# Kernel optimization log

Measured on AMD Instinct MI355X. Metric: run time of the kernel, lower is better.

The kernel has to match this reference:

```python
import jax, jax.numpy as jnp
import numpy as np

B, S, D, H = 2, 2048, 1024, 16
HD = D // H  # head_dim = 64


def setup_inputs() -> dict:
    key = jax.random.key(0)
    ks = jax.random.split(key, 9)
    scale = 0.02
    x = jax.random.normal(ks[0], (B, S, D), dtype=jnp.float32)
    wq = jax.random.normal(ks[1], (D, D), dtype=jnp.float32) * scale
    bq = jnp.zeros((D,), dtype=jnp.float32)
    wk = jax.random.normal(ks[2], (D, D), dtype=jnp.float32) * scale
    bk = jnp.zeros((D,), dtype=jnp.float32)
    wv = jax.random.normal(ks[3], (D, D), dtype=jnp.float32) * scale
    bv = jnp.zeros((D,), dtype=jnp.float32)
    wo = jax.random.normal(ks[4], (D, D), dtype=jnp.float32) * scale
    bo = jnp.zeros((D,), dtype=jnp.float32)
    # causal mask: 1.0 where key position is in the future of query position
    mask = jnp.triu(jnp.ones((S, S), dtype=jnp.float32), k=1)[None, None]  # [1,1,S,S]
    return {"x": x, "wq": wq, "bq": bq, "wk": wk, "bk": bk,
            "wv": wv, "bv": bv, "wo": wo, "bo": bo, "mask": mask}


def reference(x, wq, bq, wk, bk, wv, bv, wo, bo, mask):
    b, s, d = x.shape
    q = (x @ wq + bq).reshape(b, s, H, HD).transpose(0, 2, 1, 3)  # [b,h,s,hd]
    k = (x @ wk + bk).reshape(b, s, H, HD).transpose(0, 2, 1, 3)
    v = (x @ wv + bv).reshape(b, s, H, HD).transpose(0, 2, 1, 3)
    scores = jnp.einsum('bhqd,bhkd->bhqk', q, k) / jnp.sqrt(jnp.float32(HD))
    scores = scores + mask * (-1e9)
    probs = jax.nn.softmax(scores, axis=-1)
    out = jnp.einsum('bhqk,bhkd->bhqd', probs, v)
    out = out.transpose(0, 2, 1, 3).reshape(b, s, d)
    return out @ wo + bo
```

## Files before the change

kernel.cpp:

```cpp
#include <hip/hip_runtime.h>
#include <hip/hip_bf16.h>
#include <cstdint>

#define DEV static __device__ __forceinline__

typedef unsigned short u16t;
typedef __attribute__((ext_vector_type(4))) float f32x4;
typedef __attribute__((ext_vector_type(4))) unsigned short u16x4;
typedef __attribute__((ext_vector_type(8))) unsigned short u16x8;
typedef __attribute__((ext_vector_type(8))) __bf16 bf16x8;

DEV u16t f2bf(float f) {
  unsigned u = __builtin_bit_cast(unsigned, f);
  u += 0x7fffu + ((u >> 16) & 1u);
  return (u16t)(u >> 16);
}
DEV float bf2f(u16t h) {
  unsigned u = ((unsigned)h) << 16;
  return __builtin_bit_cast(float, u);
}

DEV void gload_lds16(const void* g, void* l) {
  __builtin_amdgcn_global_load_lds(
      (const __attribute__((address_space(1))) void*)g,
      (__attribute__((address_space(3))) void*)l, 16, 0, 0);
}

DEV bf16x8 ldsfrag(const u16t* p) {
  return __builtin_bit_cast(bf16x8, *(const u16x8*)p);
}

DEV void bsync() {
  asm volatile("" ::: "memory");
  __builtin_amdgcn_s_barrier();
  asm volatile("" ::: "memory");
}

__global__ __launch_bounds__(256) void k_convert_x(const float* __restrict__ x,
                                                   u16t* __restrict__ xb) {
  int i = (blockIdx.x * 256 + threadIdx.x) * 4;
  f32x4 v = *(const f32x4*)&x[i];
  u16x4 o;
#pragma unroll
  for (int j = 0; j < 4; ++j) o[j] = f2bf(v[j]);
  *(u16x4*)&xb[i] = o;
}

__global__ __launch_bounds__(256) void k_transw(const float* __restrict__ w0,
                                                const float* __restrict__ w1,
                                                const float* __restrict__ w2,
                                                const float* __restrict__ w3,
                                                u16t* __restrict__ qkvT,
                                                u16t* __restrict__ oT) {
  __shared__ float lds[64][68];
  int z = blockIdx.z;
  const float* W = (z == 0) ? w0 : (z == 1) ? w1 : (z == 2) ? w2 : w3;
  u16t* OUT = (z < 3) ? (qkvT + (size_t)z * 1024 * 1024) : oT;
  int k0 = blockIdx.x * 64, n0 = blockIdx.y * 64;
  int t = threadIdx.x;
  int kl = t >> 4, n4 = (t & 15) << 2;
#pragma unroll
  for (int p = 0; p < 4; ++p) {
    f32x4 v = *(const f32x4*)&W[(size_t)(k0 + kl + p * 16) * 1024 + n0 + n4];
    *(f32x4*)&lds[kl + p * 16][n4] = v;
  }
  __syncthreads();
  int nl = t >> 4, k4 = (t & 15) << 2;
#pragma unroll
  for (int p = 0; p < 4; ++p) {
    int n = nl + p * 16;
    u16x4 o;
#pragma unroll
    for (int i = 0; i < 4; ++i) o[i] = f2bf(lds[k4 + i][n]);
    *(u16x4*)&OUT[(size_t)(n0 + n) * 1024 + k0 + k4] = o;
  }
}

template <int MI, bool BF16_OUT, bool VSPLIT>
__global__ __launch_bounds__(256) void k_gemm_bt(const u16t* __restrict__ A,
                                                 const u16t* __restrict__ BT,
                                                 void* __restrict__ Cout,
                                                 const float* __restrict__ b0,
                                                 const float* __restrict__ b1,
                                                 const float* __restrict__ b2,
                                                 u16t* __restrict__ vt,
                                                 int M, int N, int K) {
  __shared__ u16t Al[2][MI * 32 * 64];
  __shared__ u16t Bl[2][128 * 64];
  const int tid = threadIdx.x;
  const int l = tid & 63;
  const int w = tid >> 6;
  const int m0 = blockIdx.x * (MI * 32), n0 = blockIdx.y * 128;
  const int wm = (w >> 1) * (MI * 16), wn = (w & 1) * 64;
  const int lm = l & 15, lh = l >> 4;
  f32x4 acc[MI][4] = {};

  auto stage = [&](int bb, int t) {
    const int k0 = t << 6;
#pragma unroll
    for (int s = 0; s < MI; ++s) {
      int c = s * 256 + tid;
      int row = c >> 3, slot = c & 7;
      int ks = k0 + (((slot ^ (row & 7)) & 7) << 3);
      gload_lds16(A + (size_t)(m0 + row) * K + ks, &Al[bb][c * 8]);
    }
#pragma unroll
    for (int s = 0; s < 4; ++s) {
      int c = s * 256 + tid;
      int row = c >> 3, slot = c & 7;
      int ks = k0 + (((slot ^ (row & 7)) & 7) << 3);
      gload_lds16(BT + (size_t)(n0 + row) * K + ks, &Bl[bb][c * 8]);
    }
  };

  const int nt = K >> 6;
  stage(0, 0);
  for (int t = 0; t < nt; ++t) {
    if (t + 1 < nt) {
      stage((t + 1) & 1, t + 1);
      if (MI == 2)
        asm volatile("s_waitcnt vmcnt(6)" ::: "memory");
      else
        asm volatile("s_waitcnt vmcnt(8)" ::: "memory");
    } else {
      asm volatile("s_waitcnt vmcnt(0)" ::: "memory");
    }
    bsync();
    const int buf = t & 1;

#pragma unroll
    for (int kk = 0; kk < 2; ++kk) {
      bf16x8 af[MI], bfr[4];
#pragma unroll
      for (int i = 0; i < MI; ++i) {
        int ra = wm + i * 16 + lm;
        int sa = (kk * 4 + lh) ^ (ra & 7);
        af[i] = ldsfrag(&Al[buf][ra * 64 + sa * 8]);
      }
#pragma unroll
      for (int i = 0; i < 4; ++i) {
        int rb = wn + i * 16 + lm;
        int sb = (kk * 4 + lh) ^ (rb & 7);
        bfr[i] = ldsfrag(&Bl[buf][rb * 64 + sb * 8]);
      }
#pragma unroll
      for (int i = 0; i < MI; ++i)
#pragma unroll
        for (int j = 0; j < 4; ++j)
          acc[i][j] = __builtin_amdgcn_mfma_f32_16x16x32_bf16(af[i], bfr[j],
                                                              acc[i][j], 0, 0, 0);
    }
    bsync();
  }

  if (!VSPLIT || (n0 + wn) < 2048) {
#pragma unroll
    for (int i = 0; i < MI; ++i) {
      int row = m0 + wm + i * 16 + (lh << 2);
#pragma unroll
      for (int j = 0; j < 4; ++j) {
        int col = n0 + wn + j * 16 + lm;
        const float* bp = (col < 1024) ? b0 : ((col < 2048) ? b1 : b2);
        float bias = bp[col & 1023];
#pragma unroll
        for (int r = 0; r < 4; ++r) {
          float v = acc[i][j][r] + bias;
          if (BF16_OUT)
            ((u16t*)Cout)[(size_t)(row + r) * N + col] = f2bf(v);
          else
            ((float*)Cout)[(size_t)(row + r) * N + col] = v;
        }
      }
    }
  } else {
#pragma unroll
    for (int i = 0; i < MI; ++i) {
      int row = m0 + wm + i * 16 + (lh << 2);
      int bidx = row >> 11, s0 = row & 2047;
#pragma unroll
      for (int j = 0; j < 4; ++j) {
        int col = n0 + wn + j * 16 + lm;
        int d = col - 2048;
        int hh = d >> 6, dd = d & 63;
        float bias = b2[d];
        u16x4 o;
#pragma unroll
        for (int r = 0; r < 4; ++r) o[r] = f2bf(acc[i][j][r] + bias);
        *(u16x4*)&vt[((size_t)((bidx * 16 + hh) * 64 + dd)) * 2048 + s0] = o;
      }
    }
  }
}

__global__ __launch_bounds__(256, 2) void k_attn(const u16t* qkv,
                                                 const u16t* __restrict__ vt,
                                                 u16t* __restrict__ outp,
                                                 u16t* scratch) {
  __shared__ u16t Kl[4096];
  __shared__ u16t Vl[4096];
  __shared__ u16t Pl[4][2][1024];
  const int tid = threadIdx.x, l = tid & 63, w = tid >> 6;
  const int lm = l & 15, lh = l >> 4;
  const int bh = blockIdx.x, b = bh >> 4, h = bh & 15;
  const int y = blockIdx.y;
  const int zone = y >> 3, j = y & 7;
  const int qt = (zone == 0) ? j : (15 - j);
  const int q0 = qt * 128;
  const int halfn = qt + 1;
  const int t0 = (zone == 2) ? halfn : 0;
  const int t1 = (zone == 1) ? halfn : (2 * qt + 2);
  const int qbase = q0 + w * 32;

  bf16x8 aq[2][2];
#pragma unroll
  for (int qm = 0; qm < 2; ++qm)
#pragma unroll
    for (int kk = 0; kk < 2; ++kk) {
      const u16t* src = qkv + (size_t)(b * 2048 + qbase + qm * 16 + lm) * 3072 +
                        h * 64 + kk * 32 + lh * 8;
      u16x8 v = *(const u16x8*)src;
      u16x8 o;
#pragma unroll
      for (int e = 0; e < 8; ++e) o[e] = f2bf(bf2f(v[e]) * 0.1803368801f);
      aq[qm][kk] = __builtin_bit_cast(bf16x8, o);
    }

  float lsum[2] = {0.f, 0.f};
  f32x4 aco[2][4] = {};
  const int qr0 = qbase + lm, qr1 = qbase + 16 + lm;

  const u16t* Kg = qkv + (size_t)b * 2048 * 3072 + 1024 + h * 64;
  const u16t* Vg = vt + (size_t)bh * 64 * 2048;

  auto stage = [&](int t) {
#pragma unroll
    for (int s = 0; s < 2; ++s) {
      int c = s * 256 + tid;
      int row = c >> 3, col = ((c & 7) ^ (row & 7)) << 3;
      gload_lds16(Kg + (size_t)(t * 64 + row) * 3072 + col, &Kl[c * 8]);
    }
#pragma unroll
    for (int s = 0; s < 2; ++s) {
      int c = s * 256 + tid;
      int row = c >> 3, col = ((c & 7) ^ (row & 7)) << 3;
      gload_lds16(Vg + (size_t)row * 2048 + t * 64 + col, &Vl[c * 8]);
    }
  };

  for (int t = t0; t < t1; ++t) {
    stage(t);
    asm volatile("s_waitcnt vmcnt(0)" ::: "memory");
    bsync();

    if (t * 64 <= qbase + 31) {
      f32x4 accs[2][4] = {};
#pragma unroll
      for (int kk = 0; kk < 2; ++kk) {
        bf16x8 ak[4];
#pragma unroll
        for (int nk = 0; nk < 4; ++nk) {
          int rk = nk * 16 + lm;
          int s16 = (kk * 4 + lh) ^ (rk & 7);
          ak[nk] = ldsfrag(&Kl[rk * 64 + s16 * 8]);
        }
        __builtin_amdgcn_s_setprio(1);
#pragma unroll
        for (int nk = 0; nk < 4; ++nk) {
          accs[0][nk] = __builtin_amdgcn_mfma_f32_16x16x32_bf16(
              ak[nk], aq[0][kk], accs[0][nk], 0, 0, 0);
          accs[1][nk] = __builtin_amdgcn_mfma_f32_16x16x32_bf16(
              ak[nk], aq[1][kk], accs[1][nk], 0, 0, 0);
        }
        __builtin_amdgcn_s_setprio(0);
      }

      if (t * 64 + 63 > qbase) {
#pragma unroll
        for (int nk = 0; nk < 4; ++nk)
#pragma unroll
          for (int r = 0; r < 4; ++r) {
            int kvpos = t * 64 + nk * 16 + lh * 4 + r;
            if (kvpos > qr0) accs[0][nk][r] = -1e30f;
            if (kvpos > qr1) accs[1][nk][r] = -1e30f;
          }
      }

#pragma unroll
      for (int qm = 0; qm < 2; ++qm) {
        u16t* Pw = &Pl[w][qm][0];
#pragma unroll
        for (int nk = 0; nk < 4; ++nk) {
          float p0 = exp2f(accs[qm][nk][0]);
          float p1 = exp2f(accs[qm][nk][1]);
          float p2 = exp2f(accs[qm][nk][2]);
          float p3 = exp2f(accs[qm][nk][3]);
          lsum[qm] += (p0 + p1) + (p2 + p3);
          unsigned wlo, whi;
          asm("v_cvt_pk_bf16_f32 %0, %1, %2" : "=v"(wlo) : "v"(p0), "v"(p1));
          asm("v_cvt_pk_bf16_f32 %0, %1, %2" : "=v"(whi) : "v"(p2), "v"(p3));
          int off = lm * 64 + ((((2 * nk + (lh >> 1)) ^ (lm & 7)) & 7) << 3) +
                    ((lh & 1) << 2);
          *(uint2*)&Pw[off] = make_uint2(wlo, whi);
        }
      }

#pragma unroll
      for (int kk = 0; kk < 2; ++kk) {
        int sp = (kk * 4 + lh) ^ (lm & 7);
        bf16x8 ap0 = ldsfrag(&Pl[w][0][lm * 64 + sp * 8]);
        bf16x8 ap1 = ldsfrag(&Pl[w][1][lm * 64 + sp * 8]);
        __builtin_amdgcn_s_setprio(1);
#pragma unroll
        for (int nd = 0; nd < 4; ++nd) {
          int rv = nd * 16 + lm;
          int sv = (kk * 4 + lh) ^ (rv & 7);
          bf16x8 bv = ldsfrag(&Vl[rv * 64 + sv * 8]);
          aco[0][nd] =
              __builtin_amdgcn_mfma_f32_16x16x32_bf16(ap0, bv, aco[0][nd], 0, 0, 0);
          aco[1][nd] =
              __builtin_amdgcn_mfma_f32_16x16x32_bf16(ap1, bv, aco[1][nd], 0, 0, 0);
        }
        __builtin_amdgcn_s_setprio(0);
      }
    }

    bsync();
  }

#pragma unroll
  for (int qm = 0; qm < 2; ++qm) {
    lsum[qm] += __shfl_xor(lsum[qm], 16);
    lsum[qm] += __shfl_xor(lsum[qm], 32);
  }

  if (zone == 0) {
#pragma unroll
    for (int qm = 0; qm < 2; ++qm) {
      float inv = 1.0f / lsum[qm];
#pragma unroll
      for (int r = 0; r < 4; ++r) {
        float ir = __shfl(inv, lh * 4 + r);
        int row = qbase + qm * 16 + lh * 4 + r;
#pragma unroll
        for (int nd = 0; nd < 4; ++nd) {
          int col = h * 64 + nd * 16 + lm;
          outp[(size_t)(b * 2048 + row) * 1024 + col] = f2bf(aco[qm][nd][r] * ir);
        }
      }
    }
  } else {
#pragma unroll
    for (int qm = 0; qm < 2; ++qm)
#pragma unroll
      for (int r = 0; r < 4; ++r) {
        int row = qbase + qm * 16 + lh * 4 + r;
#pragma unroll
        for (int nd = 0; nd < 4; ++nd) {
          int col = nd * 16 + lm;
          u16t v = f2bf(aco[qm][nd][r]);
          if (zone == 1)
            outp[(size_t)(b * 2048 + row) * 1024 + h * 64 + col] = v;
          else
            scratch[(size_t)(b * 2048 + row - 1024) * 3072 + 2048 + h * 64 + col] = v;
        }
      }
    if (l < 16) {
      float* ml0 = (float*)&scratch[(size_t)(b * 2048 + qbase + l) * 3072 + 2048];
      ml0[h * 2 + (zone - 1)] = lsum[0];
      float* ml1 =
          (float*)&scratch[(size_t)(b * 2048 + qbase + 16 + l) * 3072 + 2048];
      ml1[h * 2 + (zone - 1)] = lsum[1];
    }
  }
}

__global__ __launch_bounds__(256) void k_merge(const u16t* __restrict__ scratch,
                                               u16t* __restrict__ outp) {
  int x = blockIdx.x;
  int b = x >> 10, rr = x & 1023, row = 1024 + rr;
  int c4 = threadIdx.x * 4;
  int h = c4 >> 6;
  const float* ml = (const float*)&scratch[(size_t)(b * 2048 + row) * 3072 + 2048];
  float inv = 1.0f / (ml[h * 2] + ml[h * 2 + 1]);
  u16t* op = &outp[(size_t)(b * 2048 + row) * 1024 + c4];
  const u16t* o1 = &scratch[(size_t)(b * 2048 + rr) * 3072 + 2048 + c4];
  u16x4 a = *(const u16x4*)op;
  u16x4 bb = *(const u16x4*)o1;
  u16x4 o;
#pragma unroll
  for (int i = 0; i < 4; ++i) o[i] = f2bf((bf2f(a[i]) + bf2f(bb[i])) * inv);
  *(u16x4*)op = o;
}

extern "C" void kernel_launch(void* const* d_in, const int* in_sizes, int n_in,
                              void* d_out, int out_size, void* d_ws, size_t ws_size,
                              hipStream_t stream) {
  const float* x = (const float*)d_in[0];
  const float* wq = (const float*)d_in[1];
  const float* bq = (const float*)d_in[2];
  const float* wk = (const float*)d_in[3];
  const float* bk = (const float*)d_in[4];
  const float* wv = (const float*)d_in[5];
  const float* bv = (const float*)d_in[6];
  const float* wo = (const float*)d_in[7];
  const float* bo = (const float*)d_in[8];

  char* ws = (char*)d_ws;
  u16t* xb = (u16t*)ws;
  u16t* wqkvT = (u16t*)(ws + (8u << 20));
  u16t* woT = (u16t*)(ws + (14u << 20));
  u16t* qkv = (u16t*)(ws + (16u << 20));
  u16t* vt = (u16t*)(ws + (40u << 20));
  u16t* attn_out = xb;

  k_convert_x<<<4096, 256, 0, stream>>>(x, xb);
  k_transw<<<dim3(16, 16, 4), 256, 0, stream>>>(wq, wk, wv, wo, wqkvT, woT);
  k_gemm_bt<2, true, true><<<dim3(64, 24), 256, 0, stream>>>(
      xb, wqkvT, qkv, bq, bk, bv, vt, 4096, 3072, 1024);
  k_attn<<<dim3(32, 24), 256, 0, stream>>>(qkv, vt, attn_out, qkv);
  k_merge<<<2048, 256, 0, stream>>>(qkv, attn_out);
  k_gemm_bt<2, false, false><<<dim3(64, 8), 256, 0, stream>>>(
      attn_out, woT, d_out, bo, bo, bo, nullptr, 4096, 1024, 1024);
}
```

Measured before the change: 107.7 us.

## Add dedicated QKV GEMM kernel with 64x256 tiles and MFMA priority boost

Replaces the generic templated GEMM for the QKV projection with a specialized kernel using 64x256 block tiles (each wave computes 32x128), single-buffered LDS staging, and s_setprio around the MFMA loop. The wider N tile raises arithmetic intensity per A load and halves the grid to 768 blocks. The generic GEMM is simplified to fp32 output only. Dropping double buffering exposes global load latency each K step, and the larger accumulator footprint may reduce occupancy.

```diff
diff --git a/kernel.cpp b/kernel.cpp
--- a/kernel.cpp
+++ b/kernel.cpp
@@ -76,14 +76,100 @@
   }
 }
 
-template <int MI, bool BF16_OUT, bool VSPLIT>
+__global__ __launch_bounds__(256) void k_gemm_qkv(const u16t* __restrict__ A,
+                                                  const u16t* __restrict__ BT,
+                                                  u16t* __restrict__ Cout,
+                                                  const float* __restrict__ b0,
+                                                  const float* __restrict__ b1,
+                                                  const float* __restrict__ b2,
+                                                  u16t* __restrict__ vt) {
+  __shared__ u16t Al[64 * 64];
+  __shared__ u16t Bl[256 * 64];
+  const int tid = threadIdx.x;
+  const int l = tid & 63;
+  const int w = tid >> 6;
+  const int m0 = blockIdx.x * 64, n0 = blockIdx.y * 256;
+  const int wm = (w >> 1) * 32, wn = (w & 1) * 128;
+  const int lm = l & 15, lh = l >> 4;
+  f32x4 acc[2][8] = {};
+
+  for (int t = 0; t < 16; ++t) {
+    const int k0 = t << 6;
+#pragma unroll
+    for (int s = 0; s < 2; ++s) {
+      int c = s * 256 + tid;
+      int row = c >> 3, slot = c & 7;
+      int ks = k0 + (((slot ^ (row & 7)) & 7) << 3);
+      gload_lds16(A + (size_t)(m0 + row) * 1024 + ks, &Al[c * 8]);
+    }
+#pragma unroll
+    for (int s = 0; s < 8; ++s) {
+      int c = s * 256 + tid;
+      int row = c >> 3, slot = c & 7;
+      int ks = k0 + (((slot ^ (row & 7)) & 7) << 3);
+      gload_lds16(BT + (size_t)(n0 + row) * 1024 + ks, &Bl[c * 8]);
+    }
+    asm volatile("s_waitcnt vmcnt(0)" ::: "memory");
+    bsync();
+
+#pragma unroll
+    for (int kk = 0; kk < 2; ++kk) {
+      bf16x8 af[2], bfr[8];
+#pragma unroll
+      for (int i = 0; i < 2; ++i) {
+        int ra = wm + i * 16 + lm;
+        int sa = (kk * 4 + lh) ^ (ra & 7);
+        af[i] = ldsfrag(&Al[ra * 64 + sa * 8]);
+      }
+#pragma unroll
+      for (int j = 0; j < 8; ++j) {
+        int rb = wn + j * 16 + lm;
+        int sb = (kk * 4 + lh) ^ (rb & 7);
+        bfr[j] = ldsfrag(&Bl[rb * 64 + sb * 8]);
+      }
+      __builtin_amdgcn_s_setprio(1);
+#pragma unroll
+      for (int i = 0; i < 2; ++i)
+#pragma unroll
+        for (int j = 0; j < 8; ++j)
+          acc[i][j] = __builtin_amdgcn_mfma_f32_16x16x32_bf16(af[i], bfr[j],
+                                                              acc[i][j], 0, 0, 0);
+      __builtin_amdgcn_s_setprio(0);
+    }
+    bsync();
+  }
+
+#pragma unroll
+  for (int i = 0; i < 2; ++i) {
+    int row = m0 + wm + i * 16 + (lh << 2);
+    int bidx = row >> 11, s0 = row & 2047;
+#pragma unroll
+    for (int j = 0; j < 8; ++j) {
+      int col = n0 + wn + j * 16 + lm;
+      if (col < 2048) {
+        const float* bp = (col < 1024) ? b0 : b1;
+        float bias = bp[col & 1023];
+#pragma unroll
+        for (int r = 0; r < 4; ++r)
+          Cout[(size_t)(row + r) * 3072 + col] = f2bf(acc[i][j][r] + bias);
+      } else {
+        int d = col - 2048;
+        int hh = d >> 6, dd = d & 63;
+        float bias = b2[d];
+        u16x4 o;
+#pragma unroll
+        for (int r = 0; r < 4; ++r) o[r] = f2bf(acc[i][j][r] + bias);
+        *(u16x4*)&vt[((size_t)((bidx * 16 + hh) * 64 + dd)) * 2048 + s0] = o;
+      }
+    }
+  }
+}
+
+template <int MI>
 __global__ __launch_bounds__(256) void k_gemm_bt(const u16t* __restrict__ A,
                                                  const u16t* __restrict__ BT,
-                                                 void* __restrict__ Cout,
+                                                 float* __restrict__ Cout,
                                                  const float* __restrict__ b0,
-                                                 const float* __restrict__ b1,
-                                                 const float* __restrict__ b2,
-                                                 u16t* __restrict__ vt,
                                                  int M, int N, int K) {
   __shared__ u16t Al[2][MI * 32 * 64];
   __shared__ u16t Bl[2][128 * 64];
@@ -153,41 +239,16 @@
     bsync();
   }
 
-  if (!VSPLIT || (n0 + wn) < 2048) {
-#pragma unroll
-    for (int i = 0; i < MI; ++i) {
-      int row = m0 + wm + i * 16 + (lh << 2);
-#pragma unroll
-      for (int j = 0; j < 4; ++j) {
-        int col = n0 + wn + j * 16 + lm;
-        const float* bp = (col < 1024) ? b0 : ((col < 2048) ? b1 : b2);
-        float bias = bp[col & 1023];
-#pragma unroll
-        for (int r = 0; r < 4; ++r) {
-          float v = acc[i][j][r] + bias;
-          if (BF16_OUT)
-            ((u16t*)Cout)[(size_t)(row + r) * N + col] = f2bf(v);
-          else
-            ((float*)Cout)[(size_t)(row + r) * N + col] = v;
-        }
-      }
-    }
-  } else {
-#pragma unroll
-    for (int i = 0; i < MI; ++i) {
-      int row = m0 + wm + i * 16 + (lh << 2);
-      int bidx = row >> 11, s0 = row & 2047;
-#pragma unroll
-      for (int j = 0; j < 4; ++j) {
-        int col = n0 + wn + j * 16 + lm;
-        int d = col - 2048;
-        int hh = d >> 6, dd = d & 63;
-        float bias = b2[d];
-        u16x4 o;
-#pragma unroll
-        for (int r = 0; r < 4; ++r) o[r] = f2bf(acc[i][j][r] + bias);
-        *(u16x4*)&vt[((size_t)((bidx * 16 + hh) * 64 + dd)) * 2048 + s0] = o;
-      }
+#pragma unroll
+  for (int i = 0; i < MI; ++i) {
+    int row = m0 + wm + i * 16 + (lh << 2);
+#pragma unroll
+    for (int j = 0; j < 4; ++j) {
+      int col = n0 + wn + j * 16 + lm;
+      float bias = b0[col];
+#pragma unroll
+      for (int r = 0; r < 4; ++r)
+        Cout[(size_t)(row + r) * N + col] = acc[i][j][r] + bias;
     }
   }
 }
@@ -415,10 +476,9 @@
 
   k_convert_x<<<4096, 256, 0, stream>>>(x, xb);
   k_transw<<<dim3(16, 16, 4), 256, 0, stream>>>(wq, wk, wv, wo, wqkvT, woT);
-  k_gemm_bt<2, true, true><<<dim3(64, 24), 256, 0, stream>>>(
-      xb, wqkvT, qkv, bq, bk, bv, vt, 4096, 3072, 1024);
+  k_gemm_qkv<<<dim3(64, 12), 256, 0, stream>>>(xb, wqkvT, qkv, bq, bk, bv, vt);
   k_attn<<<dim3(32, 24), 256, 0, stream>>>(qkv, vt, attn_out, qkv);
   k_merge<<<2048, 256, 0, stream>>>(qkv, attn_out);
-  k_gemm_bt<2, false, false><<<dim3(64, 8), 256, 0, stream>>>(
-      attn_out, woT, d_out, bo, bo, bo, nullptr, 4096, 1024, 1024);
-}
+  k_gemm_bt<2><<<dim3(64, 8), 256, 0, stream>>>(attn_out, woT, (float*)d_out, bo,
+                                                4096, 1024, 1024);
+}
```

New measurement: 122.6 us. 13.9% more time.

## Keep P in registers and compute transposed PV with 16x16x16 MFMA

Applied to the files above, without the earlier changes.

The P tile no longer round-trips through shared memory. The score accumulator layout is fed straight in as the B operand of a 16x16x16 bf16 MFMA, with V as the A operand, which produces a transposed output accumulator. The epilogue then writes contiguous 4-element vectors per row, replacing the scattered scalar stores and removing the shuffle for the normaliser. In exchange it uses the smaller-K MFMA (twice as many instructions for the PV product) and narrower 8-byte V fragment reads from LDS, but drops the LDS writes and reads of P and frees that LDS space.

```diff
diff --git a/kernel.cpp b/kernel.cpp
--- a/kernel.cpp
+++ b/kernel.cpp
@@ -9,6 +9,7 @@
 typedef __attribute__((ext_vector_type(4))) unsigned short u16x4;
 typedef __attribute__((ext_vector_type(8))) unsigned short u16x8;
 typedef __attribute__((ext_vector_type(8))) __bf16 bf16x8;
+typedef __attribute__((ext_vector_type(4))) short s16x4;
 
 DEV u16t f2bf(float f) {
   unsigned u = __builtin_bit_cast(unsigned, f);
@@ -198,7 +199,6 @@
                                                  u16t* scratch) {
   __shared__ u16t Kl[4096];
   __shared__ u16t Vl[4096];
-  __shared__ u16t Pl[4][2][1024];
   const int tid = threadIdx.x, l = tid & 63, w = tid >> 6;
   const int lm = l & 15, lh = l >> 4;
   const int bh = blockIdx.x, b = bh >> 4, h = bh & 15;
@@ -226,7 +226,7 @@
     }
 
   float lsum[2] = {0.f, 0.f};
-  f32x4 aco[2][4] = {};
+  f32x4 acoT[2][4] = {};
   const int qr0 = qbase + lm, qr1 = qbase + 16 + lm;
 
   const u16t* Kg = qkv + (size_t)b * 2048 * 3072 + 1024 + h * 64;
@@ -285,9 +285,9 @@
           }
       }
 
-#pragma unroll
-      for (int qm = 0; qm < 2; ++qm) {
-        u16t* Pw = &Pl[w][qm][0];
+      s16x4 pb[2][4];
+#pragma unroll
+      for (int qm = 0; qm < 2; ++qm)
 #pragma unroll
         for (int nk = 0; nk < 4; ++nk) {
           float p0 = exp2f(accs[qm][nk][0]);
@@ -298,27 +298,26 @@
           unsigned wlo, whi;
           asm("v_cvt_pk_bf16_f32 %0, %1, %2" : "=v"(wlo) : "v"(p0), "v"(p1));
           asm("v_cvt_pk_bf16_f32 %0, %1, %2" : "=v"(whi) : "v"(p2), "v"(p3));
-          int off = lm * 64 + ((((2 * nk + (lh >> 1)) ^ (lm & 7)) & 7) << 3) +
-                    ((lh & 1) << 2);
-          *(uint2*)&Pw[off] = make_uint2(wlo, whi);
-        }
-      }
-
-#pragma unroll
-      for (int kk = 0; kk < 2; ++kk) {
-        int sp = (kk * 4 + lh) ^ (lm & 7);
-        bf16x8 ap0 = ldsfrag(&Pl[w][0][lm * 64 + sp * 8]);
-        bf16x8 ap1 = ldsfrag(&Pl[w][1][lm * 64 + sp * 8]);
+          pb[qm][nk] = __builtin_bit_cast(s16x4, make_uint2(wlo, whi));
+        }
+
+#pragma unroll
+      for (int nk = 0; nk < 4; ++nk) {
+        s16x4 av[4];
+#pragma unroll
+        for (int nd = 0; nd < 4; ++nd) {
+          int rowd = nd * 16 + lm;
+          int slot = (nk * 2 + (lh >> 1)) ^ (rowd & 7);
+          av[nd] = __builtin_bit_cast(
+              s16x4, *(const uint2*)&Vl[rowd * 64 + slot * 8 + (lh & 1) * 4]);
+        }
         __builtin_amdgcn_s_setprio(1);
 #pragma unroll
         for (int nd = 0; nd < 4; ++nd) {
-          int rv = nd * 16 + lm;
-          int sv = (kk * 4 + lh) ^ (rv & 7);
-          bf16x8 bv = ldsfrag(&Vl[rv * 64 + sv * 8]);
-          aco[0][nd] =
-              __builtin_amdgcn_mfma_f32_16x16x32_bf16(ap0, bv, aco[0][nd], 0, 0, 0);
-          aco[1][nd] =
-              __builtin_amdgcn_mfma_f32_16x16x32_bf16(ap1, bv, aco[1][nd], 0, 0, 0);
+          acoT[0][nd] = __builtin_amdgcn_mfma_f32_16x16x16bf16_1k(
+              av[nd], pb[0][nk], acoT[0][nd], 0, 0, 0);
+          acoT[1][nd] = __builtin_amdgcn_mfma_f32_16x16x16bf16_1k(
+              av[nd], pb[1][nk], acoT[1][nd], 0, 0, 0);
         }
         __builtin_amdgcn_s_setprio(0);
       }
@@ -337,33 +336,32 @@
 #pragma unroll
     for (int qm = 0; qm < 2; ++qm) {
       float inv = 1.0f / lsum[qm];
-#pragma unroll
-      for (int r = 0; r < 4; ++r) {
-        float ir = __shfl(inv, lh * 4 + r);
-        int row = qbase + qm * 16 + lh * 4 + r;
-#pragma unroll
-        for (int nd = 0; nd < 4; ++nd) {
-          int col = h * 64 + nd * 16 + lm;
-          outp[(size_t)(b * 2048 + row) * 1024 + col] = f2bf(aco[qm][nd][r] * ir);
-        }
+      int row = qbase + qm * 16 + lm;
+      u16t* base = &outp[(size_t)(b * 2048 + row) * 1024 + h * 64];
+#pragma unroll
+      for (int nd = 0; nd < 4; ++nd) {
+        u16x4 o;
+#pragma unroll
+        for (int r = 0; r < 4; ++r) o[r] = f2bf(acoT[qm][nd][r] * inv);
+        *(u16x4*)&base[nd * 16 + lh * 4] = o;
       }
     }
   } else {
 #pragma unroll
-    for (int qm = 0; qm < 2; ++qm)
-#pragma unroll
-      for (int r = 0; r < 4; ++r) {
-        int row = qbase + qm * 16 + lh * 4 + r;
-#pragma unroll
-        for (int nd = 0; nd < 4; ++nd) {
-          int col = nd * 16 + lm;
-          u16t v = f2bf(aco[qm][nd][r]);
-          if (zone == 1)
-            outp[(size_t)(b * 2048 + row) * 1024 + h * 64 + col] = v;
-          else
-            scratch[(size_t)(b * 2048 + row - 1024) * 3072 + 2048 + h * 64 + col] = v;
-        }
-      }
+    for (int qm = 0; qm < 2; ++qm) {
+      int row = qbase + qm * 16 + lm;
+      u16t* base =
+          (zone == 1)
+              ? &outp[(size_t)(b * 2048 + row) * 1024 + h * 64]
+              : &scratch[(size_t)(b * 2048 + row - 1024) * 3072 + 2048 + h * 64];
+#pragma unroll
+      for (int nd = 0; nd < 4; ++nd) {
+        u16x4 o;
+#pragma unroll
+        for (int r = 0; r < 4; ++r) o[r] = f2bf(acoT[qm][nd][r]);
+        *(u16x4*)&base[nd * 16 + lh * 4] = o;
+      }
+    }
     if (l < 16) {
       float* ml0 = (float*)&scratch[(size_t)(b * 2048 + qbase + l) * 3072 + 2048];
       ml0[h * 2 + (zone - 1)] = lsum[0];
```

Result: slower. 110.6 us (+2.7%).
